# Kernel tuning notes

Measured on AMD Instinct MI355X. Metric: run time of the kernel, lower is better.

## Reference

```python
import jax, jax.numpy as jnp
import numpy as np

D = 1024       # latent_size
LW = 16        # leaf_width
DEPTH = 8      # tree depth
NN = 2**DEPTH - 1   # internal decision nodes
NL = 2**DEPTH       # leaves
B, S = 2, 1024


def _fff(x, nw, nb, w1, b1, w2, b2, act):
    """Hard-routed Fast FeedForward (eval mode).
    x: (B,S,D); nw: (NN,D); nb: (NN,); w1: (NL,D,LW); b1: (NL,LW);
    w2: (NL,LW,D); b2: (NL,D).
    """
    node = jnp.zeros(x.shape[:2], dtype=jnp.int32)
    for _ in range(DEPTH):
        logit = jnp.einsum('bsd,bsd->bs', x, nw[node]) + nb[node]
        node = 2 * node + 1 + (logit > 0).astype(jnp.int32)
    leaf = node - NN  # (B,S) in [0, NL)
    h = act(jnp.einsum('bsd,bsdl->bsl', x, w1[leaf]) + b1[leaf])
    return jnp.einsum('bsl,bsld->bsd', h, w2[leaf]) + b2[leaf]


def _forward(x,
             q_nw, q_nb, q_w1, q_b1, q_w2, q_b2,
             k_nw, k_nb, k_w1, k_b1, k_w2, k_b2,
             v_nw, v_nb, v_w1, v_b1, v_w2, v_b2,
             f_nw, f_nb, f_w1, f_b1, f_w2, f_b2):
    # manual norm (torch std is unbiased; note original divides by sqrt(std+eps))
    mu = jnp.mean(x, -1, keepdims=True)
    sd = jnp.std(x, -1, ddof=1, keepdims=True)
    xn = (x - mu) / jnp.sqrt(sd + 1e-5)
    relu = jax.nn.relu
    q = _fff(xn, q_nw, q_nb, q_w1, q_b1, q_w2, q_b2, relu)
    k = _fff(xn, k_nw, k_nb, k_w1, k_b1, k_w2, k_b2, relu)
    v = _fff(xn, v_nw, v_nb, v_w1, v_b1, v_w2, v_b2, relu)
    att = jax.nn.softmax(jnp.einsum('bqd,bkd->bqk', q, k) / jnp.sqrt(jnp.float32(D)), axis=-1)
    y = xn + jnp.einsum('bqk,bkd->bqd', att, v)
    gelu = lambda t: jax.nn.gelu(t, approximate=False)
    return y + _fff(y, f_nw, f_nb, f_w1, f_b1, f_w2, f_b2, gelu)


def _make_fff_params(key, scale_in, scale_leaf):
    ks = jax.random.split(key, 4)
    nw = jax.random.normal(ks[0], (NN, D), jnp.float32) * scale_in
    nb = jnp.zeros((NN,), jnp.float32)
    w1 = jax.random.normal(ks[1], (NL, D, LW), jnp.float32) * scale_in
    b1 = jax.random.normal(ks[2], (NL, LW), jnp.float32) * 0.01
    w2 = jax.random.normal(ks[3], (NL, LW, D), jnp.float32) * scale_leaf
    b2 = jnp.zeros((NL, D), jnp.float32)
    return nw, nb, w1, b1, w2, b2


def setup_inputs() -> dict:
    key = jax.random.key(0)
    kx, kq, kk, kv, kf = jax.random.split(key, 5)
    s_in = 1.0 / np.sqrt(D)
    s_lf = 1.0 / np.sqrt(LW)
    inp = {"x": jax.random.normal(kx, (B, S, D), jnp.float32)}
    for name, kk_ in (("q", kq), ("k", kk), ("v", kv), ("f", kf)):
        nw, nb, w1, b1, w2, b2 = _make_fff_params(kk_, s_in, s_lf)
        inp.update({f"{name}_nw": nw, f"{name}_nb": nb, f"{name}_w1": w1,
                    f"{name}_b1": b1, f"{name}_w2": w2, f"{name}_b2": b2})
    return inp


def reference(x,
              q_nw, q_nb, q_w1, q_b1, q_w2, q_b2,
              k_nw, k_nb, k_w1, k_b1, k_w2, k_b2,
              v_nw, v_nb, v_w1, v_b1, v_w2, v_b2,
              f_nw, f_nb, f_w1, f_b1, f_w2, f_b2):
    return _forward(x,
                    q_nw, q_nb, q_w1, q_b1, q_w2, q_b2,
                    k_nw, k_nb, k_w1, k_b1, k_w2, k_b2,
                    v_nw, v_nb, v_w1, v_b1, v_w2, v_b2,
                    f_nw, f_nb, f_w1, f_b1, f_w2, f_b2)
```

## Files before the change

kernel.cpp:

```cpp
#include <hip/hip_runtime.h>
#include <hip/hip_bf16.h>
#include <math.h>

#define DD 1024
#define LWW 16
#define NNODES 255
#define NLEAF 256
#define BB 2
#define SS 1024
#define NTOK (BB*SS)
#define PLANE ((size_t)NTOK * DD)
#define MS ((size_t)1024 * 1024)

typedef short bf16x8 __attribute__((ext_vector_type(8)));
typedef float f32x4 __attribute__((ext_vector_type(4)));

#define GLOBAL_AS __attribute__((address_space(1)))
#define LDS_AS __attribute__((address_space(3)))

__device__ __forceinline__ void gld_lds16(const void* g, void* l) {
  __builtin_amdgcn_global_load_lds((const GLOBAL_AS unsigned int*)g,
                                   (LDS_AS unsigned int*)l, 16, 0, 0);
}

__device__ __forceinline__ unsigned short f2bf(float f) {
  union { float f; unsigned int u; } v; v.f = f;
  unsigned int u = v.u;
  unsigned int lsb = (u >> 16) & 1u;
  u += 0x7fffu + lsb;
  return (unsigned short)(u >> 16);
}
__device__ __forceinline__ float bf2f(unsigned short h) {
  union { unsigned int u; float f; } v; v.u = ((unsigned int)h) << 16;
  return v.f;
}
__device__ __forceinline__ void split3(float a, unsigned short& h0,
                                       unsigned short& h1, unsigned short& h2) {
  h0 = f2bf(a);
  float r = a - bf2f(h0);
  h1 = f2bf(r);
  float r2 = r - bf2f(h1);
  h2 = f2bf(r2);
}

__global__ __launch_bounds__(256) void norm_kernel(const float* __restrict__ x,
                                                   float* __restrict__ xn) {
  int tok = blockIdx.x, tid = threadIdx.x;
  const float4 v = ((const float4*)(x + (size_t)tok * DD))[tid];
  double s = (double)v.x + (double)v.y + (double)v.z + (double)v.w;
  double s2 = (double)v.x * v.x + (double)v.y * v.y + (double)v.z * v.z + (double)v.w * v.w;
  for (int o = 32; o; o >>= 1) { s += __shfl_down(s, o); s2 += __shfl_down(s2, o); }
  __shared__ double rs[4], rs2[4];
  __shared__ float stats[2];
  int wid = tid >> 6, lane = tid & 63;
  if (lane == 0) { rs[wid] = s; rs2[wid] = s2; }
  __syncthreads();
  if (tid == 0) {
    double ts = rs[0] + rs[1] + rs[2] + rs[3];
    double ts2 = rs2[0] + rs2[1] + rs2[2] + rs2[3];
    double mu = ts / DD;
    double var = (ts2 - DD * mu * mu) / (DD - 1);
    if (var < 0) var = 0;
    double sd = sqrt(var);
    stats[0] = (float)mu;
    stats[1] = (float)(1.0 / sqrt(sd + 1e-5));
  }
  __syncthreads();
  float mu = stats[0], inv = stats[1];
  float4 o;
  o.x = (v.x - mu) * inv; o.y = (v.y - mu) * inv;
  o.z = (v.z - mu) * inv; o.w = (v.w - mu) * inv;
  ((float4*)(xn + (size_t)tok * DD))[tid] = o;
}

__global__ __launch_bounds__(256) void route_kernel(
    const float* __restrict__ xin,
    const float* nw0, const float* nb0,
    const float* nw1, const float* nb1,
    const float* nw2, const float* nb2,
    int* __restrict__ leaf_arr, int* __restrict__ hist) {
  const float* nws[3] = {nw0, nw1, nw2};
  const float* nbs[3] = {nb0, nb1, nb2};
  int tr = blockIdx.y, tok = blockIdx.x;
  const float* nw = nws[tr];
  const float* nb = nbs[tr];
  int tid = threadIdx.x, wid = tid >> 6, lane = tid & 63;
  __shared__ double rs[4];
  __shared__ int nsh;
  const float4 xv = ((const float4*)(xin + (size_t)tok * DD))[tid];
  int node = 0;
  for (int step = 0; step < 8; ++step) {
    const float4 w = ((const float4*)(nw + (size_t)node * DD))[tid];
    double p = (double)xv.x * w.x + (double)xv.y * w.y + (double)xv.z * w.z + (double)xv.w * w.w;
    for (int o = 32; o; o >>= 1) p += __shfl_down(p, o);
    if (lane == 0) rs[wid] = p;
    __syncthreads();
    if (tid == 0) {
      double logit = rs[0] + rs[1] + rs[2] + rs[3] + (double)nb[node];
      nsh = (logit > 0.0) ? 1 : 0;
    }
    __syncthreads();
    node = 2 * node + 1 + nsh;
  }
  if (tid == 0) {
    int leaf = node - NNODES;
    leaf_arr[(size_t)tr * NTOK + tok] = leaf;
    atomicAdd(&hist[tr * NLEAF + leaf], 1);
  }
}

__global__ __launch_bounds__(256) void scan_kernel(const int* __restrict__ hist,
                                                   int* __restrict__ offs,
                                                   int* __restrict__ cursor, int ntree) {
  __shared__ int buf[256];
  int tid = threadIdx.x;
  for (int tr = 0; tr < ntree; ++tr) {
    int v = hist[tr * NLEAF + tid];
    buf[tid] = v;
    __syncthreads();
    int run = v;
    for (int off = 1; off < 256; off <<= 1) {
      int add = (tid >= off) ? buf[tid - off] : 0;
      __syncthreads();
      run += add;
      buf[tid] = run;
      __syncthreads();
    }
    if (tid == 0) offs[tr * (NLEAF + 1)] = 0;
    offs[tr * (NLEAF + 1) + tid + 1] = run;
    cursor[tr * NLEAF + tid] = run - v;
    __syncthreads();
  }
}

__global__ __launch_bounds__(256) void scatter_kernel(const int* __restrict__ leaf_arr,
                                                      int* __restrict__ cursor,
                                                      int* __restrict__ list,
                                                      int tree0, int ntree) {
  int tok = blockIdx.x * 256 + threadIdx.x;
  for (int tr = 0; tr < ntree; ++tr) {
    int slot = tree0 + tr;
    int leaf = leaf_arr[(size_t)slot * NTOK + tok];
    int pos = atomicAdd(&cursor[slot * NLEAF + leaf], 1);
    list[(size_t)slot * NTOK + pos] = tok;
  }
}

struct LeafW {
  const float* w1[3]; const float* b1[3]; const float* w2[3]; const float* b2[3];
  unsigned short* outs[3];
  float* out_res;
};

__global__ __launch_bounds__(256) void leafmlp_kernel(
    const float* __restrict__ xin,
    const int* __restrict__ list, const int* __restrict__ offs,
    LeafW W, int tree0, int act) {
  int ty = blockIdx.y;
  int slot = tree0 + ty;
  int leaf = blockIdx.x;
  int lo = offs[slot * (NLEAF + 1) + leaf], hi = offs[slot * (NLEAF + 1) + leaf + 1];
  if (lo >= hi) return;
  const int* L = list + (size_t)slot * NTOK;
  const float* W1 = W.w1[ty] + (size_t)leaf * DD * LWW;
  const float* B1 = W.b1[ty] + (size_t)leaf * LWW;
  const float* W2 = W.w2[ty] + (size_t)leaf * LWW * DD;
  const float* B2 = W.b2[ty] + (size_t)leaf * DD;
  unsigned short* osp = W.outs[ty];
  int tid = threadIdx.x;
  int seg = tid >> 4, col = tid & 15;

  __shared__ float xs[8][16][68];
  __shared__ float hpart[16][8][17];
  __shared__ float hs[8][16];

  f32x4 b2v = *(const f32x4*)(B2 + tid * 4);

  for (int c0 = lo; c0 < hi; c0 += 8) {
    int toks[8];
#pragma unroll
    for (int t = 0; t < 8; ++t) {
      int idx = c0 + t;
      toks[t] = (idx < hi) ? L[idx] : -1;
      if (toks[t] >= 0) {
        float4 v = ((const float4*)(xin + (size_t)toks[t] * DD))[tid];
        *(float4*)&xs[t][seg][col * 4] = v;
      } else {
        float4 z = {0.f, 0.f, 0.f, 0.f};
        *(float4*)&xs[t][seg][col * 4] = z;
      }
    }
    __syncthreads();

    float part[8];
#pragma unroll
    for (int t = 0; t < 8; ++t) part[t] = 0.f;
    const float* wp = W1 + seg * 1024 + col;
#pragma unroll 4
    for (int i = 0; i < 64; ++i) {
      float wv = wp[i * 16];
#pragma unroll
      for (int t = 0; t < 8; ++t) part[t] = fmaf(xs[t][seg][i], wv, part[t]);
    }
#pragma unroll
    for (int t = 0; t < 8; ++t) hpart[seg][t][col] = part[t];
    __syncthreads();

    if (tid < 128) {
      int t = tid >> 4, c = tid & 15;
      float h = B1[c];
#pragma unroll
      for (int s = 0; s < 16; ++s) h += hpart[s][t][c];
      if (act == 0) h = fmaxf(h, 0.f);
      else h = 0.5f * h * (1.f + erff(h * 0.70710678118654752f));
      hs[t][c] = h;
    }
    __syncthreads();

    f32x4 acc[8];
#pragma unroll
    for (int t = 0; t < 8; ++t) acc[t] = b2v;
#pragma unroll
    for (int l = 0; l < 16; ++l) {
      f32x4 wv = *(const f32x4*)(W2 + l * 1024 + tid * 4);
#pragma unroll
      for (int t = 0; t < 8; ++t) acc[t] += wv * hs[t][l];
    }
#pragma unroll
    for (int t = 0; t < 8; ++t) {
      if (toks[t] < 0) break;
      size_t off = (size_t)toks[t] * DD + tid * 4;
      if (osp) {
        ushort4 o0, o1, o2;
        split3(acc[t][0], o0.x, o1.x, o2.x);
        split3(acc[t][1], o0.y, o1.y, o2.y);
        split3(acc[t][2], o0.z, o1.z, o2.z);
        split3(acc[t][3], o0.w, o1.w, o2.w);
        *(ushort4*)(osp + off) = o0;
        *(ushort4*)(osp + PLANE + off) = o1;
        *(ushort4*)(osp + 2 * PLANE + off) = o2;
      } else {
        float4 o;
        o.x = xs[t][seg][col * 4 + 0] + acc[t][0];
        o.y = xs[t][seg][col * 4 + 1] + acc[t][1];
        o.z = xs[t][seg][col * 4 + 2] + acc[t][2];
        o.w = xs[t][seg][col * 4 + 3] + acc[t][3];
        *(float4*)(W.out_res + off) = o;
      }
    }
    __syncthreads();
  }
}

__global__ __launch_bounds__(256) void transpose_v(const unsigned short* __restrict__ v,
                                                   unsigned short* __restrict__ vt) {
  __shared__ unsigned short t[32][34];
  int b = blockIdx.z & 1, p = blockIdx.z >> 1;
  int s0 = blockIdx.x * 32, d0 = blockIdx.y * 32;
  int tx = threadIdx.x, ty = threadIdx.y;
  const unsigned short* vb = v + p * PLANE + (size_t)b * SS * DD;
  unsigned short* vtb = vt + p * PLANE + (size_t)b * DD * SS;
#pragma unroll
  for (int k = 0; k < 4; ++k) {
    int r = ty + 8 * k;
    t[r][tx] = vb[(size_t)(s0 + r) * DD + d0 + tx];
  }
  __syncthreads();
#pragma unroll
  for (int k = 0; k < 4; ++k) {
    int r = ty + 8 * k;
    vtb[(size_t)(d0 + r) * SS + s0 + tx] = t[tx][r];
  }
}

#define BKK 64
__global__ __launch_bounds__(256) void gemm_nt3(
    const unsigned short* __restrict__ A,
    const unsigned short* __restrict__ Bt,
    float* __restrict__ C,
    const float* __restrict__ addsrc,
    float scale) {
  __shared__ short As[3][64 * BKK];
  __shared__ short Bs[3][64 * BKK];
  int b = blockIdx.z;
  int m0 = blockIdx.x * 64, n0 = blockIdx.y * 64;
  int tid = threadIdx.x, lane = tid & 63, wid = tid >> 6;
  int wm = wid >> 1, wn = wid & 1;
  f32x4 acc[2][2] = {};

  int sk0 = (lane & 7) * 8;
  int srow0 = wid * 8 + (lane >> 3);
  int fr = lane & 15, fk = (lane >> 4) * 8;

  const unsigned short* Ap[3];
  const unsigned short* Bp[3];
#pragma unroll
  for (int p = 0; p < 3; ++p) {
    Ap[p] = A + p * PLANE + b * MS;
    Bp[p] = Bt + p * PLANE + b * MS;
  }

  for (int kt = 0; kt < 1024 / BKK; ++kt) {
    int kbase = kt * BKK;
#pragma unroll
    for (int p = 0; p < 3; ++p) {
#pragma unroll
      for (int r = 0; r < 2; ++r) {
        int row = r * 32 + srow0;
        gld_lds16(Ap[p] + (size_t)(m0 + row) * 1024 + kbase + sk0, &As[p][(r * 32 + wid * 8) * BKK]);
        gld_lds16(Bp[p] + (size_t)(n0 + row) * 1024 + kbase + sk0, &Bs[p][(r * 32 + wid * 8) * BKK]);
      }
    }
    __syncthreads();
#pragma unroll
    for (int kk = 0; kk < 2; ++kk) {
      bf16x8 af[3][2], bfr[3][2];
#pragma unroll
      for (int p = 0; p < 3; ++p) {
        af[p][0]  = *(const bf16x8*)&As[p][(wm * 32 + fr) * BKK + kk * 32 + fk];
        af[p][1]  = *(const bf16x8*)&As[p][(wm * 32 + 16 + fr) * BKK + kk * 32 + fk];
        bfr[p][0] = *(const bf16x8*)&Bs[p][(wn * 32 + fr) * BKK + kk * 32 + fk];
        bfr[p][1] = *(const bf16x8*)&Bs[p][(wn * 32 + 16 + fr) * BKK + kk * 32 + fk];
      }
#pragma unroll
      for (int mi = 0; mi < 2; ++mi)
#pragma unroll
        for (int ni = 0; ni < 2; ++ni) {
          acc[mi][ni] = __builtin_amdgcn_mfma_f32_16x16x32_bf16(af[2][mi], bfr[0][ni], acc[mi][ni], 0, 0, 0);
          acc[mi][ni] = __builtin_amdgcn_mfma_f32_16x16x32_bf16(af[1][mi], bfr[1][ni], acc[mi][ni], 0, 0, 0);
          acc[mi][ni] = __builtin_amdgcn_mfma_f32_16x16x32_bf16(af[0][mi], bfr[2][ni], acc[mi][ni], 0, 0, 0);
          acc[mi][ni] = __builtin_amdgcn_mfma_f32_16x16x32_bf16(af[1][mi], bfr[0][ni], acc[mi][ni], 0, 0, 0);
          acc[mi][ni] = __builtin_amdgcn_mfma_f32_16x16x32_bf16(af[0][mi], bfr[1][ni], acc[mi][ni], 0, 0, 0);
          acc[mi][ni] = __builtin_amdgcn_mfma_f32_16x16x32_bf16(af[0][mi], bfr[0][ni], acc[mi][ni], 0, 0, 0);
        }
    }
    __syncthreads();
  }

  float* Cb = C + b * MS;
  const float* Rb = addsrc ? addsrc + b * MS : nullptr;
  int crow0 = (lane >> 4) * 4, ccol = lane & 15;
#pragma unroll
  for (int mi = 0; mi < 2; ++mi)
#pragma unroll
    for (int ni = 0; ni < 2; ++ni) {
      int colg = n0 + wn * 32 + ni * 16 + ccol;
#pragma unroll
      for (int j = 0; j < 4; ++j) {
        int rowg = m0 + wm * 32 + mi * 16 + crow0 + j;
        float vv = acc[mi][ni][j] * scale;
        if (Rb) vv += Rb[(size_t)rowg * 1024 + colg];
        Cb[(size_t)rowg * 1024 + colg] = vv;
      }
    }
}

__global__ __launch_bounds__(256) void softmax_kernel(const float* __restrict__ sc,
                                                      unsigned short* __restrict__ P) {
  int row = blockIdx.x, tid = threadIdx.x;
  int wid = tid >> 6, lane = tid & 63;
  const float4 v = ((const float4*)(sc + (size_t)row * SS))[tid];
  float mx = fmaxf(fmaxf(v.x, v.y), fmaxf(v.z, v.w));
  for (int o = 32; o; o >>= 1) mx = fmaxf(mx, __shfl_down(mx, o));
  __shared__ float red[4];
  __shared__ float bres[2];
  if (lane == 0) red[wid] = mx;
  __syncthreads();
  if (tid == 0) bres[0] = fmaxf(fmaxf(red[0], red[1]), fmaxf(red[2], red[3]));
  __syncthreads();
  float m = bres[0];
  float e0 = expf(v.x - m), e1 = expf(v.y - m), e2 = expf(v.z - m), e3 = expf(v.w - m);
  float s = e0 + e1 + e2 + e3;
  for (int o = 32; o; o >>= 1) s += __shfl_down(s, o);
  if (lane == 0) red[wid] = s;
  __syncthreads();
  if (tid == 0) bres[1] = red[0] + red[1] + red[2] + red[3];
  __syncthreads();
  float inv = 1.f / bres[1];
  float p0 = e0 * inv, p1 = e1 * inv, p2 = e2 * inv, p3 = e3 * inv;
  ushort4 o0, o1, o2;
  split3(p0, o0.x, o1.x, o2.x);
  split3(p1, o0.y, o1.y, o2.y);
  split3(p2, o0.z, o1.z, o2.z);
  split3(p3, o0.w, o1.w, o2.w);
  size_t off = (size_t)row * SS + tid * 4;
  *(ushort4*)(P + off) = o0;
  *(ushort4*)(P + PLANE + off) = o1;
  *(ushort4*)(P + 2 * PLANE + off) = o2;
}

extern "C" void kernel_launch(void* const* d_in, const int* in_sizes, int n_in,
                              void* d_out, int out_size, void* d_ws, size_t ws_size,
                              hipStream_t stream) {
  const float* x = (const float*)d_in[0];
  const float* qp[6]; const float* kp[6]; const float* vp[6]; const float* fp[6];
  for (int i = 0; i < 6; ++i) {
    qp[i] = (const float*)d_in[1 + i];
    kp[i] = (const float*)d_in[7 + i];
    vp[i] = (const float*)d_in[13 + i];
    fp[i] = (const float*)d_in[19 + i];
  }
  char* ws = (char*)d_ws;
  float* xn           = (float*)(ws);
  unsigned short* qb  = (unsigned short*)(ws + ( 8 << 20));
  unsigned short* kb  = (unsigned short*)(ws + (20 << 20));
  unsigned short* vs  = (unsigned short*)(ws + (32 << 20));
  unsigned short* vt  = (unsigned short*)(ws + (44 << 20));
  float* sc           = (float*)(ws + (32 << 20));
  unsigned short* P   = (unsigned short*)(ws + ( 8 << 20));
  float* y            = (float*)(ws + (20 << 20));
  int* meta           = (int*)(ws + (56 << 20));
  int* hist           = meta;
  int* cursor         = meta + 1024;
  int* offs           = meta + 2048;
  int* leaf_arr       = meta + 4096;
  int* list           = meta + 4096 + 4 * NTOK;
  float* out          = (float*)d_out;

  hipMemsetAsync(hist, 0, 4 * NLEAF * sizeof(int), stream);
  norm_kernel<<<NTOK, 256, 0, stream>>>(x, xn);
  route_kernel<<<dim3(NTOK, 3), 256, 0, stream>>>(xn, qp[0], qp[1], kp[0], kp[1], vp[0], vp[1],
                                                  leaf_arr, hist);
  scan_kernel<<<1, 256, 0, stream>>>(hist, offs, cursor, 3);
  scatter_kernel<<<NTOK / 256, 256, 0, stream>>>(leaf_arr, cursor, list, 0, 3);

  LeafW Wqkv;
  Wqkv.w1[0] = qp[2]; Wqkv.b1[0] = qp[3]; Wqkv.w2[0] = qp[4]; Wqkv.b2[0] = qp[5];
  Wqkv.w1[1] = kp[2]; Wqkv.b1[1] = kp[3]; Wqkv.w2[1] = kp[4]; Wqkv.b2[1] = kp[5];
  Wqkv.w1[2] = vp[2]; Wqkv.b1[2] = vp[3]; Wqkv.w2[2] = vp[4]; Wqkv.b2[2] = vp[5];
  Wqkv.outs[0] = qb; Wqkv.outs[1] = kb; Wqkv.outs[2] = vs;
  Wqkv.out_res = nullptr;
  leafmlp_kernel<<<dim3(NLEAF, 3), 256, 0, stream>>>(xn, list, offs, Wqkv, 0, 0);

  transpose_v<<<dim3(32, 32, 6), dim3(32, 8), 0, stream>>>(vs, vt);
  gemm_nt3<<<dim3(16, 16, 2), 256, 0, stream>>>(qb, kb, sc, nullptr, 0.03125f);
  softmax_kernel<<<NTOK, 256, 0, stream>>>(sc, P);
  gemm_nt3<<<dim3(16, 16, 2), 256, 0, stream>>>(P, vt, y, xn, 1.0f);

  route_kernel<<<dim3(NTOK, 1), 256, 0, stream>>>(y, fp[0], fp[1], fp[0], fp[1], fp[0], fp[1],
                                                  leaf_arr + 3 * NTOK, hist + 3 * NLEAF);
  scan_kernel<<<1, 256, 0, stream>>>(hist + 3 * NLEAF, offs + 3 * (NLEAF + 1), cursor + 3 * NLEAF, 1);
  scatter_kernel<<<NTOK / 256, 256, 0, stream>>>(leaf_arr, cursor, list, 3, 1);

  LeafW Wf;
  Wf.w1[0] = fp[2]; Wf.b1[0] = fp[3]; Wf.w2[0] = fp[4]; Wf.b2[0] = fp[5];
  Wf.w1[1] = fp[2]; Wf.b1[1] = fp[3]; Wf.w2[1] = fp[4]; Wf.b2[1] = fp[5];
  Wf.w1[2] = fp[2]; Wf.b1[2] = fp[3]; Wf.w2[2] = fp[4]; Wf.b2[2] = fp[5];
  Wf.outs[0] = nullptr; Wf.outs[1] = nullptr; Wf.outs[2] = nullptr;
  Wf.out_res = out;
  leafmlp_kernel<<<dim3(NLEAF, 1), 256, 0, stream>>>(y, list, offs, Wf, 3, 1);
}
```

Baseline: 225.7 us.

## Route one token per wavefront and split leaf MLP work into 8-token chunks

```diff
diff --git a/kernel.cpp b/kernel.cpp
--- a/kernel.cpp
+++ b/kernel.cpp
@@ -11,6 +11,7 @@
 #define NTOK (BB*SS)
 #define PLANE ((size_t)NTOK * DD)
 #define MS ((size_t)1024 * 1024)
+#define MAXCHUNK 512
 
 typedef short bf16x8 __attribute__((ext_vector_type(8)));
 typedef float f32x4 __attribute__((ext_vector_type(4)));
@@ -78,31 +79,36 @@
     const float* nw0, const float* nb0,
     const float* nw1, const float* nb1,
     const float* nw2, const float* nb2,
-    int* __restrict__ leaf_arr, int* __restrict__ hist) {
+    int* __restrict__ leaf_arr, int* __restrict__ hist, int ntree) {
+  int tid = threadIdx.x, lane = tid & 63, wid = tid >> 6;
+  int gw = blockIdx.x * 4 + wid;
+  int tok = gw / ntree, tr = gw - tok * ntree;
+  if (tok >= NTOK) return;
   const float* nws[3] = {nw0, nw1, nw2};
   const float* nbs[3] = {nb0, nb1, nb2};
-  int tr = blockIdx.y, tok = blockIdx.x;
   const float* nw = nws[tr];
   const float* nb = nbs[tr];
-  int tid = threadIdx.x, wid = tid >> 6, lane = tid & 63;
-  __shared__ double rs[4];
-  __shared__ int nsh;
-  const float4 xv = ((const float4*)(xin + (size_t)tok * DD))[tid];
+  f32x4 xq[4];
+  const f32x4* xb = (const f32x4*)(xin + (size_t)tok * DD);
+#pragma unroll
+  for (int j = 0; j < 4; ++j) xq[j] = xb[lane + 64 * j];
   int node = 0;
+#pragma unroll 1
   for (int step = 0; step < 8; ++step) {
-    const float4 w = ((const float4*)(nw + (size_t)node * DD))[tid];
-    double p = (double)xv.x * w.x + (double)xv.y * w.y + (double)xv.z * w.z + (double)xv.w * w.w;
-    for (int o = 32; o; o >>= 1) p += __shfl_down(p, o);
-    if (lane == 0) rs[wid] = p;
-    __syncthreads();
-    if (tid == 0) {
-      double logit = rs[0] + rs[1] + rs[2] + rs[3] + (double)nb[node];
-      nsh = (logit > 0.0) ? 1 : 0;
-    }
-    __syncthreads();
-    node = 2 * node + 1 + nsh;
-  }
-  if (tid == 0) {
+    const f32x4* wb = (const f32x4*)(nw + (size_t)node * DD);
+    double p = 0.0;
+#pragma unroll
+    for (int j = 0; j < 4; ++j) {
+      f32x4 w = wb[lane + 64 * j];
+      p += (double)xq[j][0] * w[0] + (double)xq[j][1] * w[1] +
+           (double)xq[j][2] * w[2] + (double)xq[j][3] * w[3];
+    }
+#pragma unroll
+    for (int o = 1; o < 64; o <<= 1) p += __shfl_xor(p, o);
+    double logit = p + (double)nb[node];
+    node = 2 * node + 1 + (logit > 0.0 ? 1 : 0);
+  }
+  if (lane == 0) {
     int leaf = node - NNODES;
     leaf_arr[(size_t)tr * NTOK + tok] = leaf;
     atomicAdd(&hist[tr * NLEAF + leaf], 1);
@@ -111,12 +117,17 @@
 
 __global__ __launch_bounds__(256) void scan_kernel(const int* __restrict__ hist,
                                                    int* __restrict__ offs,
-                                                   int* __restrict__ cursor, int ntree) {
+                                                   int* __restrict__ cursor,
+                                                   int4* __restrict__ desc,
+                                                   int ntree, int tree0) {
   __shared__ int buf[256];
+  __shared__ int dcnt;
   int tid = threadIdx.x;
   for (int tr = 0; tr < ntree; ++tr) {
-    int v = hist[tr * NLEAF + tid];
+    int slot = tree0 + tr;
+    int v = hist[slot * NLEAF + tid];
     buf[tid] = v;
+    if (tid == 0) dcnt = 0;
     __syncthreads();
     int run = v;
     for (int off = 1; off < 256; off <<= 1) {
@@ -126,9 +137,19 @@
       buf[tid] = run;
       __syncthreads();
     }
-    if (tid == 0) offs[tr * (NLEAF + 1)] = 0;
-    offs[tr * (NLEAF + 1) + tid + 1] = run;
-    cursor[tr * NLEAF + tid] = run - v;
+    if (tid == 0) offs[slot * (NLEAF + 1)] = 0;
+    offs[slot * (NLEAF + 1) + tid + 1] = run;
+    cursor[slot * NLEAF + tid] = run - v;
+    if (v > 0) {
+      int k = (v + 7) >> 3;
+      int base = atomicAdd(&dcnt, k);
+      int lo = run - v;
+      for (int j = 0; j < k; ++j) {
+        int s = lo + j * 8;
+        int e = min(run, s + 8);
+        desc[slot * MAXCHUNK + base + j] = make_int4(tid, s, e, 0);
+      }
+    }
     __syncthreads();
   }
 }
@@ -154,13 +175,14 @@
 
 __global__ __launch_bounds__(256) void leafmlp_kernel(
     const float* __restrict__ xin,
-    const int* __restrict__ list, const int* __restrict__ offs,
+    const int* __restrict__ list, const int4* __restrict__ desc,
     LeafW W, int tree0, int act) {
   int ty = blockIdx.y;
   int slot = tree0 + ty;
-  int leaf = blockIdx.x;
-  int lo = offs[slot * (NLEAF + 1) + leaf], hi = offs[slot * (NLEAF + 1) + leaf + 1];
-  if (lo >= hi) return;
+  int4 dsc = desc[slot * MAXCHUNK + blockIdx.x];
+  int leaf = dsc.x;
+  if (leaf < 0) return;
+  int lo = dsc.y, hi = dsc.z;
   const int* L = list + (size_t)slot * NTOK;
   const float* W1 = W.w1[ty] + (size_t)leaf * DD * LWW;
   const float* B1 = W.b1[ty] + (size_t)leaf * LWW;
@@ -174,81 +196,85 @@
   __shared__ float hpart[16][8][17];
   __shared__ float hs[8][16];
 
+  f32x4 w2r[16];
+#pragma unroll
+  for (int l = 0; l < 16; ++l) w2r[l] = *(const f32x4*)(W2 + l * 1024 + tid * 4);
   f32x4 b2v = *(const f32x4*)(B2 + tid * 4);
 
-  for (int c0 = lo; c0 < hi; c0 += 8) {
-    int toks[8];
+  int toks[8];
+#pragma unroll
+  for (int t = 0; t < 8; ++t) {
+    int idx = lo + t;
+    toks[t] = (idx < hi) ? L[idx] : -1;
+    if (toks[t] >= 0) {
+      float4 v = ((const float4*)(xin + (size_t)toks[t] * DD))[tid];
+      *(float4*)&xs[t][seg][col * 4] = v;
+    } else {
+      float4 z = {0.f, 0.f, 0.f, 0.f};
+      *(float4*)&xs[t][seg][col * 4] = z;
+    }
+  }
+  __syncthreads();
+
+  float part[8];
+#pragma unroll
+  for (int t = 0; t < 8; ++t) part[t] = 0.f;
+  const float* wp = W1 + seg * 1024 + col;
+#pragma unroll 4
+  for (int i4 = 0; i4 < 64; i4 += 4) {
+    float w0 = wp[(i4 + 0) * 16], w1v = wp[(i4 + 1) * 16];
+    float w2v = wp[(i4 + 2) * 16], w3v = wp[(i4 + 3) * 16];
 #pragma unroll
     for (int t = 0; t < 8; ++t) {
-      int idx = c0 + t;
-      toks[t] = (idx < hi) ? L[idx] : -1;
-      if (toks[t] >= 0) {
-        float4 v = ((const float4*)(xin + (size_t)toks[t] * DD))[tid];
-        *(float4*)&xs[t][seg][col * 4] = v;
-      } else {
-        float4 z = {0.f, 0.f, 0.f, 0.f};
-        *(float4*)&xs[t][seg][col * 4] = z;
-      }
-    }
-    __syncthreads();
-
-    float part[8];
-#pragma unroll
-    for (int t = 0; t < 8; ++t) part[t] = 0.f;
-    const float* wp = W1 + seg * 1024 + col;
-#pragma unroll 4
-    for (int i = 0; i < 64; ++i) {
-      float wv = wp[i * 16];
-#pragma unroll
-      for (int t = 0; t < 8; ++t) part[t] = fmaf(xs[t][seg][i], wv, part[t]);
-    }
-#pragma unroll
-    for (int t = 0; t < 8; ++t) hpart[seg][t][col] = part[t];
-    __syncthreads();
-
-    if (tid < 128) {
-      int t = tid >> 4, c = tid & 15;
-      float h = B1[c];
-#pragma unroll
-      for (int s = 0; s < 16; ++s) h += hpart[s][t][c];
-      if (act == 0) h = fmaxf(h, 0.f);
-      else h = 0.5f * h * (1.f + erff(h * 0.70710678118654752f));
-      hs[t][c] = h;
-    }
-    __syncthreads();
-
-    f32x4 acc[8];
-#pragma unroll
-    for (int t = 0; t < 8; ++t) acc[t] = b2v;
-#pragma unroll
-    for (int l = 0; l < 16; ++l) {
-      f32x4 wv = *(const f32x4*)(W2 + l * 1024 + tid * 4);
-#pragma unroll
-      for (int t = 0; t < 8; ++t) acc[t] += wv * hs[t][l];
-    }
-#pragma unroll
-    for (int t = 0; t < 8; ++t) {
-      if (toks[t] < 0) break;
-      size_t off = (size_t)toks[t] * DD + tid * 4;
-      if (osp) {
-        ushort4 o0, o1, o2;
-        split3(acc[t][0], o0.x, o1.x, o2.x);
-        split3(acc[t][1], o0.y, o1.y, o2.y);
-        split3(acc[t][2], o0.z, o1.z, o2.z);
-        split3(acc[t][3], o0.w, o1.w, o2.w);
-        *(ushort4*)(osp + off) = o0;
-        *(ushort4*)(osp + PLANE + off) = o1;
-        *(ushort4*)(osp + 2 * PLANE + off) = o2;
-      } else {
-        float4 o;
-        o.x = xs[t][seg][col * 4 + 0] + acc[t][0];
-        o.y = xs[t][seg][col * 4 + 1] + acc[t][1];
-        o.z = xs[t][seg][col * 4 + 2] + acc[t][2];
-        o.w = xs[t][seg][col * 4 + 3] + acc[t][3];
-        *(float4*)(W.out_res + off) = o;
-      }
-    }
-    __syncthreads();
+      float4 xv4 = *(const float4*)&xs[t][seg][i4];
+      part[t] = fmaf(xv4.x, w0, fmaf(xv4.y, w1v, fmaf(xv4.z, w2v, fmaf(xv4.w, w3v, part[t]))));
+    }
+  }
+#pragma unroll
+  for (int t = 0; t < 8; ++t) hpart[seg][t][col] = part[t];
+  __syncthreads();
+
+  if (tid < 128) {
+    int t = tid >> 4, c = tid & 15;
+    float h = B1[c];
+#pragma unroll
+    for (int s = 0; s < 16; ++s) h += hpart[s][t][c];
+    if (act == 0) h = fmaxf(h, 0.f);
+    else h = 0.5f * h * (1.f + erff(h * 0.70710678118654752f));
+    hs[t][c] = h;
+  }
+  __syncthreads();
+
+  f32x4 acc[8];
+#pragma unroll
+  for (int t = 0; t < 8; ++t) acc[t] = b2v;
+#pragma unroll
+  for (int l = 0; l < 16; ++l) {
+    f32x4 wv = w2r[l];
+#pragma unroll
+    for (int t = 0; t < 8; ++t) acc[t] += wv * hs[t][l];
+  }
+#pragma unroll
+  for (int t = 0; t < 8; ++t) {
+    if (toks[t] < 0) break;
+    size_t off = (size_t)toks[t] * DD + tid * 4;
+    if (osp) {
+      ushort4 o0, o1, o2;
+      split3(acc[t][0], o0.x, o1.x, o2.x);
+      split3(acc[t][1], o0.y, o1.y, o2.y);
+      split3(acc[t][2], o0.z, o1.z, o2.z);
+      split3(acc[t][3], o0.w, o1.w, o2.w);
+      *(ushort4*)(osp + off) = o0;
+      *(ushort4*)(osp + PLANE + off) = o1;
+      *(ushort4*)(osp + 2 * PLANE + off) = o2;
+    } else {
+      float4 o;
+      o.x = xs[t][seg][col * 4 + 0] + acc[t][0];
+      o.y = xs[t][seg][col * 4 + 1] + acc[t][1];
+      o.z = xs[t][seg][col * 4 + 2] + acc[t][2];
+      o.w = xs[t][seg][col * 4 + 3] + acc[t][3];
+      *(float4*)(W.out_res + off) = o;
+    }
   }
 }
 
@@ -414,14 +440,16 @@
   int* cursor         = meta + 1024;
   int* offs           = meta + 2048;
   int* leaf_arr       = meta + 4096;
-  int* list           = meta + 4096 + 4 * NTOK;
+  int* list           = meta + 12288;
+  int4* desc          = (int4*)(meta + 20480);
   float* out          = (float*)d_out;
 
-  hipMemsetAsync(hist, 0, 4 * NLEAF * sizeof(int), stream);
+  hipMemsetAsync(hist, 0, 1024 * sizeof(int), stream);
+  hipMemsetAsync(desc, 0xFF, 4 * MAXCHUNK * sizeof(int4), stream);
   norm_kernel<<<NTOK, 256, 0, stream>>>(x, xn);
-  route_kernel<<<dim3(NTOK, 3), 256, 0, stream>>>(xn, qp[0], qp[1], kp[0], kp[1], vp[0], vp[1],
-                                                  leaf_arr, hist);
-  scan_kernel<<<1, 256, 0, stream>>>(hist, offs, cursor, 3);
+  route_kernel<<<NTOK * 3 / 4, 256, 0, stream>>>(xn, qp[0], qp[1], kp[0], kp[1], vp[0], vp[1],
+                                                 leaf_arr, hist, 3);
+  scan_kernel<<<1, 256, 0, stream>>>(hist, offs, cursor, desc, 3, 0);
   scatter_kernel<<<NTOK / 256, 256, 0, stream>>>(leaf_arr, cursor, list, 0, 3);
 
   LeafW Wqkv;
@@ -430,16 +458,16 @@
   Wqkv.w1[2] = vp[2]; Wqkv.b1[2] = vp[3]; Wqkv.w2[2] = vp[4]; Wqkv.b2[2] = vp[5];
   Wqkv.outs[0] = qb; Wqkv.outs[1] = kb; Wqkv.outs[2] = vs;
   Wqkv.out_res = nullptr;
-  leafmlp_kernel<<<dim3(NLEAF, 3), 256, 0, stream>>>(xn, list, offs, Wqkv, 0, 0);
+  leafmlp_kernel<<<dim3(MAXCHUNK, 3), 256, 0, stream>>>(xn, list, desc, Wqkv, 0, 0);
 
   transpose_v<<<dim3(32, 32, 6), dim3(32, 8), 0, stream>>>(vs, vt);
   gemm_nt3<<<dim3(16, 16, 2), 256, 0, stream>>>(qb, kb, sc, nullptr, 0.03125f);
   softmax_kernel<<<NTOK, 256, 0, stream>>>(sc, P);
   gemm_nt3<<<dim3(16, 16, 2), 256, 0, stream>>>(P, vt, y, xn, 1.0f);
 
-  route_kernel<<<dim3(NTOK, 1), 256, 0, stream>>>(y, fp[0], fp[1], fp[0], fp[1], fp[0], fp[1],
-                                                  leaf_arr + 3 * NTOK, hist + 3 * NLEAF);
-  scan_kernel<<<1, 256, 0, stream>>>(hist + 3 * NLEAF, offs + 3 * (NLEAF + 1), cursor + 3 * NLEAF, 1);
+  route_kernel<<<NTOK / 4, 256, 0, stream>>>(y, fp[0], fp[1], fp[0], fp[1], fp[0], fp[1],
+                                             leaf_arr + 3 * NTOK, hist + 3 * NLEAF, 1);
+  scan_kernel<<<1, 256, 0, stream>>>(hist, offs, cursor, desc, 1, 3);
   scatter_kernel<<<NTOK / 256, 256, 0, stream>>>(leaf_arr, cursor, list, 3, 1);
 
   LeafW Wf;
@@ -448,5 +476,5 @@
   Wf.w1[2] = fp[2]; Wf.b1[2] = fp[3]; Wf.w2[2] = fp[4]; Wf.b2[2] = fp[5];
   Wf.outs[0] = nullptr; Wf.outs[1] = nullptr; Wf.outs[2] = nullptr;
   Wf.out_res = out;
-  leafmlp_kernel<<<dim3(NLEAF, 1), 256, 0, stream>>>(y, list, offs, Wf, 3, 1);
-}
+  leafmlp_kernel<<<dim3(MAXCHUNK, 1), 256, 0, stream>>>(y, list, desc, Wf, 3, 1);
+}
```

Result: faster. 214.7 us (-4.9%).
